# Kernel tuning notes

Hardware: AMD Instinct MI355X
Metric: run time of the kernel (lower is better)

## Reference

```python
import math
import jax, jax.numpy as jnp
import numpy as np

QDEPTH = 8
WIDTH = 32
HEIGHT = 32
PIXELS = WIDTH * HEIGHT          # 1024
WIRES = int(math.ceil(math.log2(PIXELS)))  # 10, and PIXELS == 2**WIRES exactly
BATCH = 2048


def setup_inputs() -> dict:
    key = jax.random.key(0)
    k1, k2 = jax.random.split(key)
    x = jax.random.normal(k1, (BATCH, 1, WIDTH, HEIGHT), dtype=jnp.float32)
    # torch.randn(weight_shape) * 0.4
    weights = jax.random.normal(k2, (QDEPTH, WIRES, 3), dtype=jnp.float32) * 0.4
    return {"x": x, "weights": weights, "reps": 1}


def _apply_1q(s, U, wire):
    # s: (batch, 2, 2, ..., 2); apply 2x2 unitary U on qubit `wire` (axis wire+1)
    ax = wire + 1
    s = jnp.moveaxis(s, ax, -1)
    s = s @ U.T                      # new[..., i] = sum_j U[i, j] * old[..., j]
    return jnp.moveaxis(s, -1, ax)


def _apply_cnot(s, ctrl, tgt):
    # flip target bit on the control==1 half of the state
    c_ax = ctrl + 1
    t_ax = tgt + 1
    s0 = jnp.take(s, 0, axis=c_ax)
    s1 = jnp.take(s, 1, axis=c_ax)
    t = t_ax - 1 if t_ax > c_ax else t_ax
    s1 = jnp.flip(s1, axis=t)
    return jnp.stack([s0, s1], axis=c_ax)


def _rot_matrix(phi, theta, omega):
    # qml.Rot = RZ(phi) -> RY(theta) -> RZ(omega)
    c = jnp.cos(theta * 0.5)
    sn = jnp.sin(theta * 0.5)
    ep = jnp.exp(-0.5j * (phi + omega))   # e^{-i(phi+omega)/2}
    em = jnp.exp(-0.5j * (phi - omega))   # e^{-i(phi-omega)/2}
    return jnp.stack([
        jnp.stack([ep * c, -jnp.conj(em) * sn]),
        jnp.stack([em * sn, jnp.conj(ep) * c]),
    ]).astype(jnp.complex64)


def _circuit(psi, weights, reps):
    # psi: (batch, 2**WIRES) complex64 normalized state
    b = psi.shape[0]
    s = psi.reshape((b,) + (2,) * WIRES)
    w = jnp.tanh(weights)                 # qw_map.tanh
    # StronglyEntanglingLayers default ranges: r_l = l % (wires-1) + 1
    ranges = [(l % (WIRES - 1)) + 1 for l in range(QDEPTH)]
    for _ in range(reps):
        for l in range(QDEPTH):
            for q in range(WIRES):
                U = _rot_matrix(w[l, q, 0], w[l, q, 1], w[l, q, 2])
                s = _apply_1q(s, U, q)
            r = ranges[l]
            for q in range(WIRES):
                s = _apply_cnot(s, q, (q + r) % WIRES)
    return s.reshape(b, 2 ** WIRES)


def reference(x, weights, reps):
    b = x.shape[0]
    v = x.reshape(b, PIXELS)                       # b 1 w h -> b (w h)
    old_norm = jnp.linalg.norm(v, axis=-1, keepdims=True)
    psi = (v / old_norm).astype(jnp.complex64)     # real amplitudes, zero imag
    out = _circuit(psi, weights, reps)
    out = out * old_norm.astype(jnp.complex64)
    return out.reshape(b, 1, WIDTH, HEIGHT)
```

## Files before the change

### kernel.cpp

```cpp
#include <hip/hip_runtime.h>
#include <math.h>


#define WIRES   10
#define NSTATE  1024
#define QDEPTH  8
#define NBATCH  2048
#define NGATES  (QDEPTH * WIRES)

#define WS_WORDS 1280

__device__ __forceinline__ int perm_g(int j, int r) {
    for (int q = WIRES - 1; q >= 0; --q) {
        const int cb = 9 - q;
        const int tb = 9 - ((q + r) % WIRES);
        j ^= ((j >> cb) & 1) << tb;
    }
    return j;
}

__global__ __launch_bounds__(1024) void qprep(
    const float* __restrict__ weights, float* __restrict__ ws)
{
    const int tid = threadIdx.x;
    if (tid < NGATES) {
        const float phi   = tanhf(weights[tid * 3 + 0]);
        const float theta = tanhf(weights[tid * 3 + 1]);
        const float omega = tanhf(weights[tid * 3 + 2]);
        const float c  = cosf(theta * 0.5f);
        const float sn = sinf(theta * 0.5f);
        const float a  = 0.5f * (phi + omega);
        const float bb = 0.5f * (phi - omega);
        const float ca = cosf(a),  sa = sinf(a);
        const float cb = cosf(bb), sb = sinf(bb);
        ws[tid * 8 + 0] =  ca * c;  ws[tid * 8 + 1] = -sa * c;
        ws[tid * 8 + 2] = -cb * sn; ws[tid * 8 + 3] = -sb * sn;
        ws[tid * 8 + 4] =  cb * sn; ws[tid * 8 + 5] = -sb * sn;
        ws[tid * 8 + 6] =  ca * c;  ws[tid * 8 + 7] =  sa * c;
    }
    int* wsI = (int*)ws;
    if (tid >= 128 && tid < 256) {
        const int e = tid - 128, l = e >> 4, t = e & 15;
        const int j = perm_g(t, (l % (WIRES - 1)) + 1);
        wsI[640 + e] = ((j & 15) << 6) | (j >> 4);
    }
    if (tid >= 256 && tid < 768) {
        const int e = tid - 256, l = e >> 6, v = e & 63;
        const int j = perm_g(v << 4, (l % (WIRES - 1)) + 1);
        wsI[768 + e] = ((j & 15) << 6) | (j >> 4);
    }
}

__global__ __launch_bounds__(64) void qsim_wave(
    const float* __restrict__ x,
    const float* __restrict__ ws,
    float* __restrict__ out,
    const int interleaved)
{
    __shared__ float lre[NSTATE];
    __shared__ float lim[NSTATE];
    const int lane = threadIdx.x;
    const int b    = blockIdx.x;
    const int* __restrict__ wsI = (const int*)ws;

    float re[16], im[16];

    const float4* __restrict__ x4 =
        (const float4*)(x + ((size_t)b << 10) + (lane << 4));
#pragma unroll
    for (int k = 0; k < 4; ++k) {
        const float4 v = x4[k];
        re[4*k+0] = v.x; re[4*k+1] = v.y; re[4*k+2] = v.z; re[4*k+3] = v.w;
        im[4*k+0] = 0.f; im[4*k+1] = 0.f; im[4*k+2] = 0.f; im[4*k+3] = 0.f;
    }

    for (int l = 0; l < QDEPTH; ++l) {
        const float* __restrict__ gw = ws + l * 80;

#pragma unroll
        for (int bb = 0; bb < 4; ++bb) {
            const float* __restrict__ u = gw + (9 - bb) * 8;
            const float u00r = u[0], u00i = u[1], u01r = u[2], u01i = u[3];
            const float u10r = u[4], u10i = u[5], u11r = u[6], u11i = u[7];
#pragma unroll
            for (int t0 = 0; t0 < 16; ++t0) {
                if (t0 & (1 << bb)) continue;
                const int t1 = t0 | (1 << bb);
                const float a0r = re[t0], a0i = im[t0];
                const float a1r = re[t1], a1i = im[t1];
                re[t0] = u00r*a0r - u00i*a0i + u01r*a1r - u01i*a1i;
                im[t0] = u00r*a0i + u00i*a0r + u01r*a1i + u01i*a1r;
                re[t1] = u10r*a0r - u10i*a0i + u11r*a1r - u11i*a1i;
                im[t1] = u10r*a0i + u10i*a0r + u11r*a1i + u11i*a1r;
            }
        }

#pragma unroll
        for (int j = 0; j < 6; ++j) {
            const float* __restrict__ u = gw + (5 - j) * 8;
            const float u00r = u[0], u00i = u[1], u01r = u[2], u01i = u[3];
            const float u10r = u[4], u10i = u[5], u11r = u[6], u11i = u[7];
            const bool hi = (lane >> j) & 1;
            const float c0r = hi ? u11r : u00r, c0i = hi ? u11i : u00i;
            const float c1r = hi ? u10r : u01r, c1i = hi ? u10i : u01i;
#pragma unroll
            for (int t = 0; t < 16; ++t) {
                const float pr = __shfl_xor(re[t], 1 << j, 64);
                const float pi = __shfl_xor(im[t], 1 << j, 64);
                const float sr = re[t], si = im[t];
                re[t] = c0r*sr - c0i*si + c1r*pr - c1i*pi;
                im[t] = c0r*si + c0i*sr + c1r*pi + c1i*pr;
            }
        }

#pragma unroll
        for (int t = 0; t < 16; ++t) {
            lre[t * 64 + lane] = re[t];
            lim[t * 64 + lane] = im[t];
        }
        const int ga = wsI[768 + l * 64 + lane];
#pragma unroll
        for (int t = 0; t < 16; ++t) {
            const int a = ga ^ wsI[640 + l * 16 + t];
            re[t] = lre[a];
            im[t] = lim[a];
        }
    }

    if (interleaved) {
        float2* __restrict__ o2 = (float2*)out;
#pragma unroll
        for (int t = 0; t < 16; ++t)
            o2[((size_t)b << 10) + (lane << 4) + t] = make_float2(re[t], im[t]);
    } else {
        float4* __restrict__ o4 = (float4*)(out + ((size_t)b << 10) + (lane << 4));
#pragma unroll
        for (int k = 0; k < 4; ++k)
            o4[k] = make_float4(re[4*k+0], re[4*k+1], re[4*k+2], re[4*k+3]);
    }
}

__global__ __launch_bounds__(256) void qcircuit_kernel(
    const float* __restrict__ x, const float* __restrict__ weights,
    float* __restrict__ out, const int interleaved)
{
    __shared__ float s_re[NSTATE];
    __shared__ float s_im[NSTATE];
    __shared__ float s_g[NGATES][8];
    const int tid = threadIdx.x;
    const int b   = blockIdx.x;
    if (tid < NGATES) {
        const float phi   = tanhf(weights[tid * 3 + 0]);
        const float theta = tanhf(weights[tid * 3 + 1]);
        const float omega = tanhf(weights[tid * 3 + 2]);
        const float c  = cosf(theta * 0.5f);
        const float sn = sinf(theta * 0.5f);
        const float a  = 0.5f * (phi + omega);
        const float bb = 0.5f * (phi - omega);
        const float ca = cosf(a),  sa = sinf(a);
        const float cb = cosf(bb), sb = sinf(bb);
        s_g[tid][0] =  ca * c;  s_g[tid][1] = -sa * c;
        s_g[tid][2] = -cb * sn; s_g[tid][3] = -sb * sn;
        s_g[tid][4] =  cb * sn; s_g[tid][5] = -sb * sn;
        s_g[tid][6] =  ca * c;  s_g[tid][7] =  sa * c;
    }
#pragma unroll
    for (int k = 0; k < 4; ++k) {
        const int i = tid + 256 * k;
        s_re[i] = x[b * NSTATE + i];
        s_im[i] = 0.0f;
    }
    __syncthreads();
    for (int l = 0; l < QDEPTH; ++l) {
        for (int q = 0; q < WIRES; ++q) {
            const int gi = l * WIRES + q;
            const float u00r = s_g[gi][0], u00i = s_g[gi][1];
            const float u01r = s_g[gi][2], u01i = s_g[gi][3];
            const float u10r = s_g[gi][4], u10i = s_g[gi][5];
            const float u11r = s_g[gi][6], u11i = s_g[gi][7];
            const int sh = 9 - q;
            const int m  = 1 << sh;
#pragma unroll
            for (int k = 0; k < 2; ++k) {
                const int p  = tid + 256 * k;
                const int i0 = ((p >> sh) << (sh + 1)) | (p & (m - 1));
                const int i1 = i0 | m;
                const float a0r = s_re[i0], a0i = s_im[i0];
                const float a1r = s_re[i1], a1i = s_im[i1];
                s_re[i0] = u00r*a0r - u00i*a0i + u01r*a1r - u01i*a1i;
                s_im[i0] = u00r*a0i + u00i*a0r + u01r*a1i + u01i*a1r;
                s_re[i1] = u10r*a0r - u10i*a0i + u11r*a1r - u11i*a1i;
                s_im[i1] = u10r*a0i + u10i*a0r + u11r*a1i + u11i*a1r;
            }
            __syncthreads();
        }
        const int r = (l % (WIRES - 1)) + 1;
        float vr[4], vi[4];
#pragma unroll
        for (int k = 0; k < 4; ++k) {
            const int i = tid + 256 * k;
            const int j = perm_g(i, r);
            vr[k] = s_re[j]; vi[k] = s_im[j];
        }
        __syncthreads();
#pragma unroll
        for (int k = 0; k < 4; ++k) {
            const int i = tid + 256 * k;
            s_re[i] = vr[k]; s_im[i] = vi[k];
        }
        __syncthreads();
    }
    if (interleaved) {
#pragma unroll
        for (int k = 0; k < 4; ++k) {
            const int i  = tid + 256 * k;
            const int fi = 2 * (b * NSTATE + i);
            out[fi + 0] = s_re[i];
            out[fi + 1] = s_im[i];
        }
    } else {
#pragma unroll
        for (int k = 0; k < 4; ++k) {
            const int i = tid + 256 * k;
            out[b * NSTATE + i] = s_re[i];
        }
    }
}

extern "C" void kernel_launch(void* const* d_in, const int* in_sizes, int n_in,
                              void* d_out, int out_size, void* d_ws, size_t ws_size,
                              hipStream_t stream) {
    const float* x       = (const float*)d_in[0];
    const float* weights = (const float*)d_in[1];
    float* out = (float*)d_out;
    const int interleaved = (out_size >= 2 * NBATCH * NSTATE) ? 1 : 0;

    if (ws_size >= WS_WORDS * sizeof(float)) {
        float* ws = (float*)d_ws;
        qprep<<<1, 1024, 0, stream>>>(weights, ws);
        qsim_wave<<<NBATCH, 64, 0, stream>>>(x, ws, out, interleaved);
    } else {
        qcircuit_kernel<<<NBATCH, 256, 0, stream>>>(x, weights, out, interleaved);
    }
}
```

Baseline: 120.5 us.

## Replace cross-lane shuffles with padded shared-memory transposes for high-qubit gates

Instead of applying the six cross-lane qubit gates with pairs of wavefront shuffles per amplitude, the kernel now transposes the state through a padded float2 shared buffer twice per layer, so that every gate runs as a register-local 2x2 update. The CNOT permutation index is computed in-kernel from XOR-linear bit images rather than loaded from precomputed workspace tables, which shrinks the prep kernel and the workspace. This removes 192 shuffles per layer in exchange for extra LDS round trips, relying on a stride-17 padding to avoid bank conflicts.

```diff
diff --git a/kernel.cpp b/kernel.cpp
--- a/kernel.cpp
+++ b/kernel.cpp
@@ -7,10 +7,10 @@
 #define QDEPTH  8
 #define NBATCH  2048
 #define NGATES  (QDEPTH * WIRES)
-
-#define WS_WORDS 1280
+#define WS_WORDS 640
 
 __device__ __forceinline__ int perm_g(int j, int r) {
+#pragma unroll
     for (int q = WIRES - 1; q >= 0; --q) {
         const int cb = 9 - q;
         const int tb = 9 - ((q + r) % WIRES);
@@ -19,7 +19,7 @@
     return j;
 }
 
-__global__ __launch_bounds__(1024) void qprep(
+__global__ __launch_bounds__(128) void qprep(
     const float* __restrict__ weights, float* __restrict__ ws)
 {
     const int tid = threadIdx.x;
@@ -38,18 +38,25 @@
         ws[tid * 8 + 4] =  cb * sn; ws[tid * 8 + 5] = -sb * sn;
         ws[tid * 8 + 6] =  ca * c;  ws[tid * 8 + 7] =  sa * c;
     }
-    int* wsI = (int*)ws;
-    if (tid >= 128 && tid < 256) {
-        const int e = tid - 128, l = e >> 4, t = e & 15;
-        const int j = perm_g(t, (l % (WIRES - 1)) + 1);
-        wsI[640 + e] = ((j & 15) << 6) | (j >> 4);
-    }
-    if (tid >= 256 && tid < 768) {
-        const int e = tid - 256, l = e >> 6, v = e & 63;
-        const int j = perm_g(v << 4, (l % (WIRES - 1)) + 1);
-        wsI[768 + e] = ((j & 15) << 6) | (j >> 4);
-    }
-}
+}
+
+#define APPLY_LOCAL(uptr, mask)                                               \
+    {                                                                         \
+        const float* __restrict__ u = (uptr);                                 \
+        const float u00r = u[0], u00i = u[1], u01r = u[2], u01i = u[3];       \
+        const float u10r = u[4], u10i = u[5], u11r = u[6], u11i = u[7];       \
+        _Pragma("unroll")                                                     \
+        for (int t0 = 0; t0 < 16; ++t0) {                                     \
+            if (t0 & (mask)) continue;                                        \
+            const int t1 = t0 | (mask);                                       \
+            const float a0r = re[t0], a0i = im[t0];                           \
+            const float a1r = re[t1], a1i = im[t1];                           \
+            re[t0] = u00r*a0r - u00i*a0i + u01r*a1r - u01i*a1i;               \
+            im[t0] = u00r*a0i + u00i*a0r + u01r*a1i + u01i*a1r;               \
+            re[t1] = u10r*a0r - u10i*a0i + u11r*a1r - u11i*a1i;               \
+            im[t1] = u10r*a0i + u10i*a0r + u11r*a1i + u11i*a1r;               \
+        }                                                                     \
+    }
 
 __global__ __launch_bounds__(64) void qsim_wave(
     const float* __restrict__ x,
@@ -57,13 +64,15 @@
     float* __restrict__ out,
     const int interleaved)
 {
-    __shared__ float lre[NSTATE];
-    __shared__ float lim[NSTATE];
+    __shared__ float2 buf[1087];
     const int lane = threadIdx.x;
     const int b    = blockIdx.x;
-    const int* __restrict__ wsI = (const int*)ws;
 
     float re[16], im[16];
+
+    const int pA = 17 * lane;
+    const int pB = 17 * (lane & 48) + (lane & 15);
+    const int pC = 17 * (lane >> 2) + (lane & 3);
 
     const float4* __restrict__ x4 =
         (const float4*)(x + ((size_t)b << 10) + (lane << 4));
@@ -77,53 +86,59 @@
     for (int l = 0; l < QDEPTH; ++l) {
         const float* __restrict__ gw = ws + l * 80;
 
-#pragma unroll
-        for (int bb = 0; bb < 4; ++bb) {
-            const float* __restrict__ u = gw + (9 - bb) * 8;
-            const float u00r = u[0], u00i = u[1], u01r = u[2], u01i = u[3];
-            const float u10r = u[4], u10i = u[5], u11r = u[6], u11i = u[7];
-#pragma unroll
-            for (int t0 = 0; t0 < 16; ++t0) {
-                if (t0 & (1 << bb)) continue;
-                const int t1 = t0 | (1 << bb);
-                const float a0r = re[t0], a0i = im[t0];
-                const float a1r = re[t1], a1i = im[t1];
-                re[t0] = u00r*a0r - u00i*a0i + u01r*a1r - u01i*a1i;
-                im[t0] = u00r*a0i + u00i*a0r + u01r*a1i + u01i*a1r;
-                re[t1] = u10r*a0r - u10i*a0i + u11r*a1r - u11i*a1i;
-                im[t1] = u10r*a0i + u10i*a0r + u11r*a1i + u11i*a1r;
-            }
-        }
-
-#pragma unroll
-        for (int j = 0; j < 6; ++j) {
-            const float* __restrict__ u = gw + (5 - j) * 8;
-            const float u00r = u[0], u00i = u[1], u01r = u[2], u01i = u[3];
-            const float u10r = u[4], u10i = u[5], u11r = u[6], u11i = u[7];
-            const bool hi = (lane >> j) & 1;
-            const float c0r = hi ? u11r : u00r, c0i = hi ? u11i : u00i;
-            const float c1r = hi ? u10r : u01r, c1i = hi ? u10i : u01i;
-#pragma unroll
-            for (int t = 0; t < 16; ++t) {
-                const float pr = __shfl_xor(re[t], 1 << j, 64);
-                const float pi = __shfl_xor(im[t], 1 << j, 64);
-                const float sr = re[t], si = im[t];
-                re[t] = c0r*sr - c0i*si + c1r*pr - c1i*pi;
-                im[t] = c0r*si + c0i*sr + c1r*pi + c1i*pr;
-            }
-        }
-
+        APPLY_LOCAL(gw + 9*8, 1)
+        APPLY_LOCAL(gw + 8*8, 2)
+        APPLY_LOCAL(gw + 7*8, 4)
+        APPLY_LOCAL(gw + 6*8, 8)
+
+#pragma unroll
+        for (int t = 0; t < 16; ++t)
+            buf[pA + t] = make_float2(re[t], im[t]);
 #pragma unroll
         for (int t = 0; t < 16; ++t) {
-            lre[t * 64 + lane] = re[t];
-            lim[t * 64 + lane] = im[t];
-        }
-        const int ga = wsI[768 + l * 64 + lane];
+            const float2 v = buf[pB + 17 * t];
+            re[t] = v.x; im[t] = v.y;
+        }
+
+        APPLY_LOCAL(gw + 5*8, 1)
+        APPLY_LOCAL(gw + 4*8, 2)
+        APPLY_LOCAL(gw + 3*8, 4)
+        APPLY_LOCAL(gw + 2*8, 8)
+
+#pragma unroll
+        for (int t = 0; t < 16; ++t)
+            buf[pB + 17 * t] = make_float2(re[t], im[t]);
 #pragma unroll
         for (int t = 0; t < 16; ++t) {
-            const int a = ga ^ wsI[640 + l * 16 + t];
-            re[t] = lre[a];
-            im[t] = lim[a];
+            const float2 v = buf[pC + 272 * (t >> 2) + 4 * (t & 3)];
+            re[t] = v.x; im[t] = v.y;
+        }
+
+        APPLY_LOCAL(gw + 1*8, 4)
+        APPLY_LOCAL(gw + 0*8, 8)
+
+#pragma unroll
+        for (int t = 0; t < 16; ++t)
+            buf[pC + 272 * (t >> 2) + 4 * (t & 3)] = make_float2(re[t], im[t]);
+
+        const int r = (l % (WIRES - 1)) + 1;
+        int Gl[6], Gt[4];
+#pragma unroll
+        for (int jb = 0; jb < 6; ++jb) Gl[jb] = perm_g(1 << (4 + jb), r);
+#pragma unroll
+        for (int tb = 0; tb < 4; ++tb) Gt[tb] = perm_g(1 << tb, r);
+        int glx = 0;
+#pragma unroll
+        for (int jb = 0; jb < 6; ++jb)
+            glx ^= ((lane >> jb) & 1) ? Gl[jb] : 0;
+
+#pragma unroll
+        for (int t = 0; t < 16; ++t) {
+            const int gt = ((t & 1) ? Gt[0] : 0) ^ ((t & 2) ? Gt[1] : 0) ^
+                           ((t & 4) ? Gt[2] : 0) ^ ((t & 8) ? Gt[3] : 0);
+            const int j = glx ^ gt;
+            const float2 v = buf[j + (j >> 4)];
+            re[t] = v.x; im[t] = v.y;
         }
     }
 
@@ -237,7 +252,7 @@
 
     if (ws_size >= WS_WORDS * sizeof(float)) {
         float* ws = (float*)d_ws;
-        qprep<<<1, 1024, 0, stream>>>(weights, ws);
+        qprep<<<1, 128, 0, stream>>>(weights, ws);
         qsim_wave<<<NBATCH, 64, 0, stream>>>(x, ws, out, interleaved);
     } else {
         qcircuit_kernel<<<NBATCH, 256, 0, stream>>>(x, weights, out, interleaved);
```

Result: slower. 125.4 us (+4.1%).
